# Kernel optimization log

Hardware: AMD Instinct MI355X
Metric: run time of the kernel (lower is better)

Reference implementation:

```python
import jax, jax.numpy as jnp
import numpy as np

HIDDEN = 768
NUM_HEADS = 8
NUM_CELLS = 16384
MAX_HDRS = 8
NUM_HEADERS = 512
LN_EPS = 1e-5


def setup_inputs() -> dict:
    key = jax.random.key(0)
    ks = jax.random.split(key, 16)
    s = 0.02
    D = HIDDEN
    return {
        "cell_value_embeddings": jax.random.normal(ks[0], (NUM_CELLS, D), jnp.float32),
        "header_embeddings": jax.random.normal(ks[1], (NUM_HEADERS, D), jnp.float32),
        "cell_to_header_map": jax.random.randint(ks[2], (NUM_CELLS, MAX_HDRS), 0, NUM_HEADERS),
        "cell_positions": jax.random.randint(ks[3], (NUM_CELLS, 2), 0, 100),
        # nn.MultiheadAttention params
        "in_proj_w": jax.random.normal(ks[4], (3 * D, D), jnp.float32) * s,
        "in_proj_b": jnp.zeros((3 * D,), jnp.float32),
        "out_w": jax.random.normal(ks[5], (D, D), jnp.float32) * s,
        "out_b": jnp.zeros((D,), jnp.float32),
        # positional embedding tables
        "row_emb": jax.random.normal(ks[6], (100, D), jnp.float32) * s,
        "col_emb": jax.random.normal(ks[7], (100, D), jnp.float32) * s,
        # fusion: Linear(2D->D) + LayerNorm
        "fus_w": jax.random.normal(ks[8], (D, 2 * D), jnp.float32) * s,
        "fus_b": jnp.zeros((D,), jnp.float32),
        "ln_g": jnp.ones((D,), jnp.float32),
        "ln_b": jnp.zeros((D,), jnp.float32),
    }


def _forward(cell_value_embeddings, header_embeddings, in_proj_w, in_proj_b,
             out_w, out_b, row_emb, col_emb, fus_w, fus_b, ln_g, ln_b,
             cell_to_header_map, cell_positions):
    N, D = cell_value_embeddings.shape
    H = cell_to_header_map.shape[1]
    nh, dh = NUM_HEADS, D // NUM_HEADS
    scale = 1.0 / (dh ** 0.5)

    pos = jnp.clip(cell_positions, 0, 99)
    cwp = cell_value_embeddings + row_emb[pos[:, 0]] + col_emb[pos[:, 1]]  # [N,D]

    ids = cell_to_header_map
    mask = ids >= 0                                   # [N,H] valid header slots
    hg = header_embeddings[jnp.where(mask, ids, 0)]   # [N,H,D] gathered K/V inputs

    Wq, Wk, Wv = jnp.split(in_proj_w, 3, axis=0)
    bq, bk, bv = jnp.split(in_proj_b, 3)
    q = (cwp @ Wq.T + bq).reshape(N, nh, dh)          # [N,a,d]
    k = (hg @ Wk.T + bk).reshape(N, H, nh, dh)        # [N,k,a,d]
    v = (hg @ Wv.T + bv).reshape(N, H, nh, dh)

    scores = jnp.einsum('nad,nkad->nak', q, k) * scale          # [N,a,k]
    scores = jnp.where(mask[:, None, :], scores, -1e9)
    attn = jax.nn.softmax(scores, axis=-1)
    attn = jnp.where(mask[:, None, :], attn, 0.0)
    ctx = jnp.einsum('nak,nkad->nad', attn, v).reshape(N, D)
    att_out = ctx @ out_w.T + out_b                    # [N,D]

    comb = jnp.concatenate([cwp, att_out], axis=-1)    # [N,2D]
    h = comb @ fus_w.T + fus_b
    mu = jnp.mean(h, axis=-1, keepdims=True)
    var = jnp.mean((h - mu) ** 2, axis=-1, keepdims=True)
    h = (h - mu) * jax.lax.rsqrt(var + LN_EPS) * ln_g + ln_b
    fused = jax.nn.relu(h)

    has = jnp.any(mask, axis=-1)                       # cells with >=1 valid header
    enriched = jnp.where(has[:, None], fused, cwp)
    weights = jnp.where(mask, attn.mean(axis=1), 0.0)  # head-averaged attn [N,H]
    return enriched, weights


def reference(cell_value_embeddings, header_embeddings, cell_to_header_map,
              cell_positions, in_proj_w, in_proj_b, out_w, out_b, row_emb,
              col_emb, fus_w, fus_b, ln_g, ln_b):
    return _forward(cell_value_embeddings, header_embeddings, in_proj_w,
                    in_proj_b, out_w, out_b, row_emb, col_emb, fus_w, fus_b,
                    ln_g, ln_b, cell_to_header_map, cell_positions)
```

## Files before the change

kernel.cpp:

```cpp
#include <hip/hip_runtime.h>
#include <hip/hip_bf16.h>

#define NCELLS 16384
#define DIM    768
#define NHEADS 8
#define DHEAD  96
#define MAXH   8
#define ND     (NCELLS * DIM)


using bf16 = __hip_bfloat16;
typedef short  short8  __attribute__((ext_vector_type(8)));
typedef short  short4v __attribute__((ext_vector_type(4)));
typedef float  floatx4 __attribute__((ext_vector_type(4)));

__device__ inline short f2b(float f) {
    bf16 h = __float2bfloat16(f);
    unsigned short u; __builtin_memcpy(&u, &h, 2); return (short)u;
}

__device__ inline short8 ld8(const float* p) {
    floatx4 a = *reinterpret_cast<const floatx4*>(p);
    floatx4 b = *reinterpret_cast<const floatx4*>(p + 4);
    short8 o;
#pragma unroll
    for (int i = 0; i < 4; ++i) { o[i] = f2b(a[i]); o[i + 4] = f2b(b[i]); }
    return o;
}

__device__ inline short8 cwp8(const float* ce, const float* re, const float* co,
                              int row, int pr, int pc, int off) {
    floatx4 a0 = *reinterpret_cast<const floatx4*>(ce + (size_t)row * DIM + off);
    floatx4 a1 = *reinterpret_cast<const floatx4*>(ce + (size_t)row * DIM + off + 4);
    floatx4 b0 = *reinterpret_cast<const floatx4*>(re + (size_t)pr * DIM + off);
    floatx4 b1 = *reinterpret_cast<const floatx4*>(re + (size_t)pr * DIM + off + 4);
    floatx4 c0 = *reinterpret_cast<const floatx4*>(co + (size_t)pc * DIM + off);
    floatx4 c1 = *reinterpret_cast<const floatx4*>(co + (size_t)pc * DIM + off + 4);
    short8 o;
#pragma unroll
    for (int i = 0; i < 4; ++i) {
        o[i]     = f2b(a0[i] + b0[i] + c0[i]);
        o[i + 4] = f2b(a1[i] + b1[i] + c1[i]);
    }
    return o;
}

template <int DUAL, int COUT>
__global__ __launch_bounds__(256) void gemm_bf(
    const bf16* __restrict__ A, const bf16* __restrict__ A2,
    const bf16* __restrict__ W, int ldw,
    const float* __restrict__ bias,
    float* __restrict__ Cf, bf16* __restrict__ Cb, int K)
{
    __shared__ short As[128 * 72];
    __shared__ short Bs[128 * 72];
    const int tid = threadIdx.x, wave = tid >> 6, lane = tid & 63;
    const int id = blockIdx.x;
    const int m0 = (id & 127) * 128;
    const int n0 = (id >> 7) * 128;
    const int wr = (wave & 1) * 64, wc = (wave >> 1) * 64;
    const int fr = lane & 15, g = lane >> 4;
    const int sr = tid >> 3, sc = (tid & 7) * 8;

    floatx4 acc[16];
#pragma unroll
    for (int i = 0; i < 16; ++i) acc[i] = (floatx4){0.f, 0.f, 0.f, 0.f};

    for (int k0 = 0; k0 < K; k0 += 64) {
        const bf16* Ak; int ka;
        if (!DUAL || k0 < DIM) { Ak = A;  ka = k0; }
        else                   { Ak = A2; ka = k0 - DIM; }
        short8 rA[4], rB[4];
#pragma unroll
        for (int i = 0; i < 4; ++i) {
            const int r = i * 32 + sr;
            rA[i] = *reinterpret_cast<const short8*>(Ak + (size_t)(m0 + r) * DIM + ka + sc);
            rB[i] = *reinterpret_cast<const short8*>(W  + (size_t)(n0 + r) * ldw + k0 + sc);
        }
        __syncthreads();
#pragma unroll
        for (int i = 0; i < 4; ++i) {
            const int r = i * 32 + sr;
            *reinterpret_cast<short8*>(&As[r * 72 + sc]) = rA[i];
            *reinterpret_cast<short8*>(&Bs[r * 72 + sc]) = rB[i];
        }
        __syncthreads();

#pragma unroll
        for (int kk = 0; kk < 2; ++kk) {
            short8 af[4], bfv[4];
#pragma unroll
            for (int i = 0; i < 4; ++i) {
                af[i]  = *reinterpret_cast<const short8*>(&As[(wr + i * 16 + fr) * 72 + kk * 32 + g * 8]);
                bfv[i] = *reinterpret_cast<const short8*>(&Bs[(wc + i * 16 + fr) * 72 + kk * 32 + g * 8]);
            }
#pragma unroll
            for (int i = 0; i < 4; ++i)
#pragma unroll
                for (int j = 0; j < 4; ++j)
                    acc[i * 4 + j] = __builtin_amdgcn_mfma_f32_16x16x32_bf16(
                        af[i], bfv[j], acc[i * 4 + j], 0, 0, 0);
        }
    }

    const int col_l = lane & 15, row_q = g * 4;
#pragma unroll
    for (int j = 0; j < 4; ++j) {
        const int col = n0 + wc + j * 16 + col_l;
        const float bv = bias[col];
#pragma unroll
        for (int i = 0; i < 4; ++i) {
#pragma unroll
            for (int r = 0; r < 4; ++r) {
                const int row = m0 + wr + i * 16 + row_q + r;
                const float v = acc[i * 4 + j][r] + bv;
                if (COUT == 0) Cf[(size_t)row * DIM + col] = v;
                else           Cb[(size_t)row * DIM + col] = __float2bfloat16(v);
            }
        }
    }
}

__global__ __launch_bounds__(256) void cwp_b_kernel(
    const float* __restrict__ ce, const int* __restrict__ pos,
    const float* __restrict__ re, const float* __restrict__ co,
    bf16* __restrict__ dst)
{
    const int cell = blockIdx.x;
    int pr = pos[cell * 2 + 0]; pr = min(max(pr, 0), 99);
    int pc = pos[cell * 2 + 1]; pc = min(max(pc, 0), 99);
    const float* a = ce + (size_t)cell * DIM;
    const float* b = re + (size_t)pr * DIM;
    const float* c = co + (size_t)pc * DIM;
    bf16* o = dst + (size_t)cell * DIM;
#pragma unroll
    for (int i = 0; i < 3; ++i) {
        const int d = threadIdx.x + i * 256;
        o[d] = __float2bfloat16(a[d] + b[d] + c[d]);
    }
}

__global__ __launch_bounds__(256) void cvt_kernel(
    const float* __restrict__ src, bf16* __restrict__ dst, int n4)
{
    const int i = blockIdx.x * 256 + threadIdx.x;
    if (i >= n4) return;
    floatx4 v = *reinterpret_cast<const floatx4*>(src + (size_t)i * 4);
    short4v o;
#pragma unroll
    for (int j = 0; j < 4; ++j) o[j] = f2b(v[j]);
    *reinterpret_cast<short4v*>((short*)dst + (size_t)i * 4) = o;
}

__global__ __launch_bounds__(256) void gemm_hkv(
    const float* __restrict__ A, int lda,
    const float* __restrict__ W, int ldw,
    const float* __restrict__ bias,
    bf16* __restrict__ C, int ldc, int K)
{
    __shared__ short As[64 * 40];
    __shared__ short Bs[64 * 40];
    const int tid = threadIdx.x, wave = tid >> 6, lane = tid & 63;
    const int m0 = blockIdx.x * 64, n0 = blockIdx.y * 64;
    const int lr = tid >> 2, lc = (tid & 3) * 8;
    const int fr = lane & 15, fk = (lane >> 4) * 8;

    floatx4 acc[4];
#pragma unroll
    for (int i = 0; i < 4; ++i) acc[i] = (floatx4){0.f, 0.f, 0.f, 0.f};

    for (int k0 = 0; k0 < K; k0 += 32) {
        short8 av = ld8(A + (size_t)(m0 + lr) * lda + k0 + lc);
        short8 wv = ld8(W + (size_t)(n0 + lr) * ldw + k0 + lc);
        __syncthreads();
        *reinterpret_cast<short8*>(&As[lr * 40 + lc]) = av;
        *reinterpret_cast<short8*>(&Bs[lr * 40 + lc]) = wv;
        __syncthreads();
        short8 af = *reinterpret_cast<const short8*>(&As[(wave * 16 + fr) * 40 + fk]);
#pragma unroll
        for (int t = 0; t < 4; ++t) {
            short8 bfv = *reinterpret_cast<const short8*>(&Bs[(t * 16 + fr) * 40 + fk]);
            acc[t] = __builtin_amdgcn_mfma_f32_16x16x32_bf16(af, bfv, acc[t], 0, 0, 0);
        }
    }
    const int col_l = lane & 15, row_q = (lane >> 4) * 4;
#pragma unroll
    for (int t = 0; t < 4; ++t) {
        const int col = n0 + t * 16 + col_l;
        const float bv = bias[col];
#pragma unroll
        for (int r = 0; r < 4; ++r) {
            const int row = m0 + wave * 16 + row_q + r;
            C[(size_t)row * ldc + col] = __float2bfloat16(acc[t][r] + bv);
        }
    }
}

__global__ __launch_bounds__(256) void attn_b_kernel(
    const bf16* __restrict__ q, bf16* __restrict__ ctx,
    const bf16* __restrict__ HKV, const int* __restrict__ map,
    float* __restrict__ wout)
{
    const int cell = blockIdx.x;
    const int t = threadIdx.x;
    __shared__ float qs[DIM];
    __shared__ float sc[64];
    __shared__ float at[64];
    __shared__ int   ids[MAXH];
    __shared__ float msk[MAXH];

    if (t < MAXH) {
        int id = map[cell * MAXH + t];
        msk[t] = (id >= 0) ? 1.f : 0.f;
        ids[t] = (id >= 0) ? id : 0;
    }
#pragma unroll
    for (int i = 0; i < 3; ++i) {
        const int d = t + i * 256;
        qs[d] = __bfloat162float(q[(size_t)cell * DIM + d]);
    }
    __syncthreads();

    if (t < 64) {
        const int a = t >> 3, j = t & 7;
        const bf16* kp = HKV + (size_t)ids[j] * 1536 + a * DHEAD;
        float s = 0.f;
        for (int d = 0; d < DHEAD; ++d)
            s += qs[a * DHEAD + d] * __bfloat162float(kp[d]);
        s *= 0.10206207261596577f;
        sc[t] = (msk[j] != 0.f) ? s : -1e9f;
    }
    __syncthreads();

    if (t < NHEADS) {
        float m = -3e38f;
        for (int j = 0; j < MAXH; ++j) m = fmaxf(m, sc[t * 8 + j]);
        float e[MAXH]; float sum = 0.f;
        for (int j = 0; j < MAXH; ++j) { e[j] = expf(sc[t * 8 + j] - m); sum += e[j]; }
        const float inv = 1.f / sum;
        for (int j = 0; j < MAXH; ++j)
            at[t * 8 + j] = (msk[j] != 0.f) ? e[j] * inv : 0.f;
    }
    __syncthreads();

    if (t < MAXH) {
        float s = 0.f;
        for (int a = 0; a < NHEADS; ++a) s += at[a * 8 + t];
        wout[(size_t)cell * MAXH + t] = s * 0.125f;
    }

#pragma unroll
    for (int i = 0; i < 3; ++i) {
        const int d = t + i * 256;
        const int a = d / DHEAD;
        float s = 0.f;
#pragma unroll
        for (int j = 0; j < MAXH; ++j)
            s += at[a * 8 + j] * __bfloat162float(HKV[(size_t)ids[j] * 1536 + DIM + d]);
        ctx[(size_t)cell * DIM + d] = __float2bfloat16(s);
    }
}

__global__ __launch_bounds__(256) void ln_kernel(
    float* io, const int* __restrict__ map,
    const float* __restrict__ ce, const int* __restrict__ pos,
    const float* __restrict__ re, const float* __restrict__ co,
    const float* __restrict__ g, const float* __restrict__ b)
{
    const int cell = blockIdx.x;
    const int t = threadIdx.x;
    __shared__ float rs[256], rq[256];
    __shared__ int hasf;
    if (t == 0) hasf = 0;

    float* hp = io + (size_t)cell * DIM;
    float v[3];
    float s = 0.f, q2 = 0.f;
#pragma unroll
    for (int i = 0; i < 3; ++i) {
        v[i] = hp[t + i * 256];
        s += v[i]; q2 += v[i] * v[i];
    }
    rs[t] = s; rq[t] = q2;
    __syncthreads();
    if (t < MAXH && map[cell * MAXH + t] >= 0) hasf = 1;
    for (int off = 128; off > 0; off >>= 1) {
        if (t < off) { rs[t] += rs[t + off]; rq[t] += rq[t + off]; }
        __syncthreads();
    }
    const float mu  = rs[0] * (1.f / 768.f);
    const float var = rq[0] * (1.f / 768.f) - mu * mu;
    const float inv = rsqrtf(var + 1e-5f);

    if (hasf) {
#pragma unroll
        for (int i = 0; i < 3; ++i) {
            const int d = t + i * 256;
            float val = (v[i] - mu) * inv * g[d] + b[d];
            hp[d] = fmaxf(val, 0.f);
        }
    } else {
        int pr = pos[cell * 2 + 0]; pr = min(max(pr, 0), 99);
        int pc = pos[cell * 2 + 1]; pc = min(max(pc, 0), 99);
#pragma unroll
        for (int i = 0; i < 3; ++i) {
            const int d = t + i * 256;
            hp[d] = ce[(size_t)cell * DIM + d] + re[(size_t)pr * DIM + d]
                  + co[(size_t)pc * DIM + d];
        }
    }
}

template <int AMODE, int CMODE>
__global__ __launch_bounds__(256) void gemm128(
    const float* A, int lda, const bf16* A2,
    const float* __restrict__ ce, const float* __restrict__ re,
    const float* __restrict__ co, const int* __restrict__ pos,
    const float* __restrict__ W, int ldw,
    const float* __restrict__ bias,
    float* Cf, bf16* Cb, int ldc, int K)
{
    __shared__ short As[128 * 40];
    __shared__ short Bs[128 * 40];
    const int tid = threadIdx.x, wave = tid >> 6, lane = tid & 63;
    const int m0 = blockIdx.x * 128, n0 = blockIdx.y * 128;
    const int wr = (wave & 1) * 64;
    const int wc = (wave >> 1) * 64;
    const int fr = lane & 15, fk = (lane >> 4) * 8;
    const int sr = tid >> 1;
    const int sk = (tid & 1) * 16;

    int pr = 0, pc = 0;
    if (AMODE != 0) {
        const int row = m0 + sr;
        pr = pos[row * 2 + 0]; pr = min(max(pr, 0), 99);
        pc = pos[row * 2 + 1]; pc = min(max(pc, 0), 99);
    }

    floatx4 acc[16];
#pragma unroll
    for (int i = 0; i < 16; ++i) acc[i] = (floatx4){0.f, 0.f, 0.f, 0.f};

    for (int k0 = 0; k0 < K; k0 += 32) {
        short8 a_lo, a_hi;
        if (AMODE == 0) {
            a_lo = ld8(A + (size_t)(m0 + sr) * lda + k0 + sk);
            a_hi = ld8(A + (size_t)(m0 + sr) * lda + k0 + sk + 8);
        } else if (AMODE == 1 || k0 < DIM) {
            a_lo = cwp8(ce, re, co, m0 + sr, pr, pc, k0 + sk);
            a_hi = cwp8(ce, re, co, m0 + sr, pr, pc, k0 + sk + 8);
        } else {
            a_lo = *reinterpret_cast<const short8*>(A2 + (size_t)(m0 + sr) * DIM + (k0 - DIM) + sk);
            a_hi = *reinterpret_cast<const short8*>(A2 + (size_t)(m0 + sr) * DIM + (k0 - DIM) + sk + 8);
        }
        short8 b_lo = ld8(W + (size_t)(n0 + sr) * ldw + k0 + sk);
        short8 b_hi = ld8(W + (size_t)(n0 + sr) * ldw + k0 + sk + 8);

        __syncthreads();
        *reinterpret_cast<short8*>(&As[sr * 40 + sk])     = a_lo;
        *reinterpret_cast<short8*>(&As[sr * 40 + sk + 8]) = a_hi;
        *reinterpret_cast<short8*>(&Bs[sr * 40 + sk])     = b_lo;
        *reinterpret_cast<short8*>(&Bs[sr * 40 + sk + 8]) = b_hi;
        __syncthreads();

        short8 af[4], bfv[4];
#pragma unroll
        for (int i = 0; i < 4; ++i) {
            af[i]  = *reinterpret_cast<const short8*>(&As[(wr + i * 16 + fr) * 40 + fk]);
            bfv[i] = *reinterpret_cast<const short8*>(&Bs[(wc + i * 16 + fr) * 40 + fk]);
        }
#pragma unroll
        for (int i = 0; i < 4; ++i)
#pragma unroll
            for (int j = 0; j < 4; ++j)
                acc[i * 4 + j] = __builtin_amdgcn_mfma_f32_16x16x32_bf16(
                    af[i], bfv[j], acc[i * 4 + j], 0, 0, 0);
    }

    const int col_l = lane & 15, row_q = (lane >> 4) * 4;
#pragma unroll
    for (int j = 0; j < 4; ++j) {
        const int col = n0 + wc + j * 16 + col_l;
        const float bv = bias[col];
#pragma unroll
        for (int i = 0; i < 4; ++i) {
#pragma unroll
            for (int r = 0; r < 4; ++r) {
                const int row = m0 + wr + i * 16 + row_q + r;
                const float v = acc[i * 4 + j][r] + bv;
                if (CMODE == 0) Cf[(size_t)row * ldc + col] = v;
                else            Cb[(size_t)row * ldc + col] = __float2bfloat16(v);
            }
        }
    }
}

__global__ __launch_bounds__(256) void attn_kernel(
    float* io, const bf16* __restrict__ HKV, const int* __restrict__ map,
    float* __restrict__ wout)
{
    const int cell = blockIdx.x;
    const int t = threadIdx.x;
    __shared__ float qs[DIM];
    __shared__ float sc[64];
    __shared__ float at[64];
    __shared__ int   ids[MAXH];
    __shared__ float msk[MAXH];

    if (t < MAXH) {
        int id = map[cell * MAXH + t];
        msk[t] = (id >= 0) ? 1.f : 0.f;
        ids[t] = (id >= 0) ? id : 0;
    }
    for (int d = t; d < DIM; d += 256)
        qs[d] = io[(size_t)cell * DIM + d];
    __syncthreads();

    if (t < 64) {
        const int a = t >> 3, j = t & 7;
        const bf16* kp = HKV + (size_t)ids[j] * 1536 + a * DHEAD;
        float s = 0.f;
        for (int d = 0; d < DHEAD; ++d)
            s += qs[a * DHEAD + d] * __bfloat162float(kp[d]);
        s *= 0.10206207261596577f;
        sc[t] = (msk[j] != 0.f) ? s : -1e9f;
    }
    __syncthreads();

    if (t < NHEADS) {
        float m = -3e38f;
        for (int j = 0; j < MAXH; ++j) m = fmaxf(m, sc[t * 8 + j]);
        float e[MAXH]; float sum = 0.f;
        for (int j = 0; j < MAXH; ++j) { e[j] = expf(sc[t * 8 + j] - m); sum += e[j]; }
        const float inv = 1.f / sum;
        for (int j = 0; j < MAXH; ++j)
            at[t * 8 + j] = (msk[j] != 0.f) ? e[j] * inv : 0.f;
    }
    __syncthreads();

    if (t < MAXH) {
        float s = 0.f;
        for (int a = 0; a < NHEADS; ++a) s += at[a * 8 + t];
        wout[(size_t)cell * MAXH + t] = s * 0.125f;
    }

    for (int d = t; d < DIM; d += 256) {
        const int a = d / DHEAD;
        float s = 0.f;
#pragma unroll
        for (int j = 0; j < MAXH; ++j)
            s += at[a * 8 + j] * __bfloat162float(HKV[(size_t)ids[j] * 1536 + DIM + d]);
        io[(size_t)cell * DIM + d] = s;
    }
}

extern "C" void kernel_launch(void* const* d_in, const int* in_sizes, int n_in,
                              void* d_out, int out_size, void* d_ws, size_t ws_size,
                              hipStream_t stream) {
    (void)in_sizes; (void)n_in; (void)out_size;

    const float* cell_emb  = (const float*)d_in[0];
    const float* hdr_emb   = (const float*)d_in[1];
    const int*   map       = (const int*)d_in[2];
    const int*   pos       = (const int*)d_in[3];
    const float* in_proj_w = (const float*)d_in[4];
    const float* in_proj_b = (const float*)d_in[5];
    const float* out_w     = (const float*)d_in[6];
    const float* out_b     = (const float*)d_in[7];
    const float* row_emb   = (const float*)d_in[8];
    const float* col_emb   = (const float*)d_in[9];
    const float* fus_w     = (const float*)d_in[10];
    const float* fus_b     = (const float*)d_in[11];
    const float* ln_g      = (const float*)d_in[12];
    const float* ln_b      = (const float*)d_in[13];
    float* out = (float*)d_out;

    char* ws = (char*)d_ws;
    bf16* HKV    = (bf16*)ws;
    bf16* att_b  = (bf16*)(ws + 1572864);
    bf16* cwp_b  = (bf16*)(ws + 26738688);
    bf16* Wq_b   = (bf16*)(ws + 51904512);
    bf16* Wo_b   = (bf16*)(ws + 53084160);
    bf16* Wf_b   = (bf16*)(ws + 54263808);
    bf16* q_b    = (bf16*)d_out;
    bf16* ctx_b  = (bf16*)((char*)d_out + 25165824);

    gemm_hkv<<<dim3(8, 24), 256, 0, stream>>>(
        hdr_emb, DIM, in_proj_w + (size_t)DIM * DIM, DIM, in_proj_b + DIM,
        HKV, 1536, DIM);

    if (ws_size >= 56623104) {
        cwp_b_kernel<<<NCELLS, 256, 0, stream>>>(cell_emb, pos, row_emb, col_emb, cwp_b);
        cvt_kernel<<<(589824 / 4 + 255) / 256, 256, 0, stream>>>(in_proj_w, Wq_b, 589824 / 4);
        cvt_kernel<<<(589824 / 4 + 255) / 256, 256, 0, stream>>>(out_w, Wo_b, 589824 / 4);
        cvt_kernel<<<(1179648 / 4 + 255) / 256, 256, 0, stream>>>(fus_w, Wf_b, 1179648 / 4);

        gemm_bf<0, 1><<<768, 256, 0, stream>>>(
            cwp_b, nullptr, Wq_b, DIM, in_proj_b, nullptr, q_b, DIM);

        attn_b_kernel<<<NCELLS, 256, 0, stream>>>(q_b, ctx_b, HKV, map, out + ND);

        gemm_bf<0, 1><<<768, 256, 0, stream>>>(
            ctx_b, nullptr, Wo_b, DIM, out_b, nullptr, att_b, DIM);

        gemm_bf<1, 0><<<768, 256, 0, stream>>>(
            cwp_b, att_b, Wf_b, 1536, fus_b, out, nullptr, 1536);
    } else {
        bf16* att_bf = (bf16*)(ws + 1572864);
        gemm128<1, 0><<<dim3(NCELLS / 128, DIM / 128), 256, 0, stream>>>(
            nullptr, 0, nullptr, cell_emb, row_emb, col_emb, pos,
            in_proj_w, DIM, in_proj_b, out, nullptr, DIM, DIM);
        attn_kernel<<<NCELLS, 256, 0, stream>>>(out, HKV, map, out + ND);
        gemm128<0, 1><<<dim3(NCELLS / 128, DIM / 128), 256, 0, stream>>>(
            out, DIM, nullptr, nullptr, nullptr, nullptr, nullptr,
            out_w, DIM, out_b, nullptr, att_bf, DIM, DIM);
        gemm128<2, 0><<<dim3(NCELLS / 128, DIM / 128), 256, 0, stream>>>(
            nullptr, 0, att_bf, cell_emb, row_emb, col_emb, pos,
            fus_w, 1536, fus_b, out, nullptr, DIM, 1536);
    }

    ln_kernel<<<NCELLS, 256, 0, stream>>>(out, map, cell_emb, pos,
                                          row_emb, col_emb, ln_g, ln_b);
}
```

Measured before the change: 353.4 us.

## Load GEMM tiles directly to LDS with XOR-swizzled layout

Result: faster. 321.8 us (-9.0%).

```diff
diff --git a/kernel.cpp b/kernel.cpp
--- a/kernel.cpp
+++ b/kernel.cpp
@@ -45,6 +45,12 @@
     return o;
 }
 
+__device__ __forceinline__ void cp16(const void* g, void* l) {
+    __builtin_amdgcn_global_load_lds(
+        (const __attribute__((address_space(1))) void*)g,
+        (__attribute__((address_space(3))) void*)l, 16, 0, 0);
+}
+
 template <int DUAL, int COUT>
 __global__ __launch_bounds__(256) void gemm_bf(
     const bf16* __restrict__ A, const bf16* __restrict__ A2,
@@ -52,15 +58,17 @@
     const float* __restrict__ bias,
     float* __restrict__ Cf, bf16* __restrict__ Cb, int K)
 {
-    __shared__ short As[128 * 72];
-    __shared__ short Bs[128 * 72];
+    __shared__ short As[128 * 64];
+    __shared__ short Bs[128 * 64];
     const int tid = threadIdx.x, wave = tid >> 6, lane = tid & 63;
     const int id = blockIdx.x;
     const int m0 = (id & 127) * 128;
     const int n0 = (id >> 7) * 128;
     const int wr = (wave & 1) * 64, wc = (wave >> 1) * 64;
-    const int fr = lane & 15, g = lane >> 4;
-    const int sr = tid >> 3, sc = (tid & 7) * 8;
+    const int fr = lane & 15, kg = lane >> 4;
+
+    const int srow = lane >> 3;
+    const int scol = (lane & 7) ^ srow;
 
     floatx4 acc[16];
 #pragma unroll
@@ -70,19 +78,16 @@
         const bf16* Ak; int ka;
         if (!DUAL || k0 < DIM) { Ak = A;  ka = k0; }
         else                   { Ak = A2; ka = k0 - DIM; }
-        short8 rA[4], rB[4];
+
+        __syncthreads();
 #pragma unroll
         for (int i = 0; i < 4; ++i) {
-            const int r = i * 32 + sr;
-            rA[i] = *reinterpret_cast<const short8*>(Ak + (size_t)(m0 + r) * DIM + ka + sc);
-            rB[i] = *reinterpret_cast<const short8*>(W  + (size_t)(n0 + r) * ldw + k0 + sc);
-        }
-        __syncthreads();
-#pragma unroll
-        for (int i = 0; i < 4; ++i) {
-            const int r = i * 32 + sr;
-            *reinterpret_cast<short8*>(&As[r * 72 + sc]) = rA[i];
-            *reinterpret_cast<short8*>(&Bs[r * 72 + sc]) = rB[i];
+            const int c = i * 4 + wave;
+            const int row = c * 8 + srow;
+            cp16(Ak + (size_t)(m0 + row) * DIM + ka + scol * 8,
+                 &As[c * 512 + lane * 8]);
+            cp16(W  + (size_t)(n0 + row) * ldw + k0 + scol * 8,
+                 &Bs[c * 512 + lane * 8]);
         }
         __syncthreads();
 
@@ -91,8 +96,9 @@
             short8 af[4], bfv[4];
 #pragma unroll
             for (int i = 0; i < 4; ++i) {
-                af[i]  = *reinterpret_cast<const short8*>(&As[(wr + i * 16 + fr) * 72 + kk * 32 + g * 8]);
-                bfv[i] = *reinterpret_cast<const short8*>(&Bs[(wc + i * 16 + fr) * 72 + kk * 32 + g * 8]);
+                const int sa = ((kk * 4 + kg) ^ (fr & 7)) * 8;
+                af[i]  = *reinterpret_cast<const short8*>(&As[(wr + i * 16 + fr) * 64 + sa]);
+                bfv[i] = *reinterpret_cast<const short8*>(&Bs[(wc + i * 16 + fr) * 64 + sa]);
             }
 #pragma unroll
             for (int i = 0; i < 4; ++i)
@@ -103,7 +109,7 @@
         }
     }
 
-    const int col_l = lane & 15, row_q = g * 4;
+    const int col_l = lane & 15, row_q = kg * 4;
 #pragma unroll
     for (int j = 0; j < 4; ++j) {
         const int col = n0 + wc + j * 16 + col_l;
```
